# Kernel tuning notes

Measured on AMD Instinct MI355X. Metric: run time of the kernel, lower is better.

The kernel has to match this reference:

```python
import jax, jax.numpy as jnp
import numpy as np

B = 32768
IN = 2
H = 512
OUT = 1
OM = 128   # output_module_size
HG = 128   # halt_gate_size
MAX_ITER = 32
EPS = 1e-3


def _w(k, shape, fan_in):
    bound = 1.0 / np.sqrt(fan_in)
    return jax.random.uniform(k, shape, jnp.float32, -bound, bound)


def setup_inputs() -> dict:
    key = jax.random.key(0)
    ks = jax.random.split(key, 32)
    d = {"x": jax.random.normal(ks[0], (B, IN), jnp.float32)}
    # four LSTM gates: input Linear(IN,H) and hidden Linear(H,H), each with bias
    names = ["i", "f", "c", "o"]
    for j, g in enumerate(names):
        d[f"W{g}_x"] = _w(ks[1 + 4 * j], (IN, H), IN)
        d[f"b{g}_x"] = _w(ks[2 + 4 * j], (H,), IN)
        d[f"W{g}_h"] = _w(ks[3 + 4 * j], (H, H), H)
        d[f"b{g}_h"] = _w(ks[4 + 4 * j], (H,), H)
    # halt gate: Linear(H,HG) -> ReLU -> Linear(HG,1) -> Sigmoid
    d["halt_W1"] = _w(ks[17], (H, HG), H)
    d["halt_b1"] = _w(ks[18], (HG,), H)
    d["halt_W2"] = _w(ks[19], (HG, 1), HG)
    d["halt_b2"] = _w(ks[20], (1,), HG)
    # output module: Linear(H,OM) -> ReLU -> Linear(OM,OM) -> Linear(OM,OUT) -> Sigmoid
    d["out_W1"] = _w(ks[21], (H, OM), H)
    d["out_b1"] = _w(ks[22], (OM,), H)
    d["out_W2"] = _w(ks[23], (OM, OM), OM)
    d["out_b2"] = _w(ks[24], (OM,), OM)
    d["out_W3"] = _w(ks[25], (OM, OUT), OM)
    d["out_b3"] = _w(ks[26], (OUT,), OM)
    return d


def _act_forward(x, Wi_x, bi_x, Wi_h, bi_h, Wf_x, bf_x, Wf_h, bf_h,
                 Wc_x, bc_x, Wc_h, bc_h, Wo_x, bo_x, Wo_h, bo_h,
                 halt_W1, halt_b1, halt_W2, halt_b2,
                 out_W1, out_b1, out_W2, out_b2, out_W3, out_b3):
    b = x.shape[0]
    # input projections are iteration-invariant: precompute once
    xi = x @ Wi_x + bi_x
    xf = x @ Wf_x + bf_x
    xc = x @ Wc_x + bc_x
    xo = x @ Wo_x + bo_x

    def step(carry, t):
        state, cell, p_sum, active, acc = carry
        i_g = jax.nn.sigmoid(xi + state @ Wi_h + bi_h)
        f_g = jax.nn.sigmoid(xf + state @ Wf_h + bf_h)
        c_g = jnp.tanh(xc + state @ Wc_h + bc_h)
        o_g = jax.nn.sigmoid(xo + state @ Wo_h + bo_h)
        am = active[:, None]
        new_cell = jnp.where(am, f_g * cell + i_g * c_g, cell)
        new_state = jnp.where(am, o_g * jnp.tanh(new_cell), state)
        # output head (inactive rows contribute zero weight below)
        h1 = jax.nn.relu(new_state @ out_W1 + out_b1)
        out = jax.nn.sigmoid((h1 @ out_W2 + out_b2) @ out_W3 + out_b3)  # [B,OUT]
        # halt probability
        hh = jax.nn.relu(new_state @ halt_W1 + halt_b1)
        halt = jax.nn.sigmoid(hh @ halt_W2 + halt_b2)[:, 0]  # [B]
        halt = jnp.where(active, halt, 0.0)
        p_new = p_sum + halt
        is_last = t == (MAX_ITER - 1)
        finished = (p_new >= 1.0 - EPS) | is_last
        adj = active & finished
        halt_adj = jnp.where(adj, halt + (1.0 - p_new), halt)
        p_new = jnp.where(adj, 1.0, p_new)
        acc = acc + out * halt_adj[:, None]
        active_new = active & jnp.logical_not(finished)
        return (new_state, new_cell, p_new, active_new, acc), None

    init = (
        jnp.zeros((b, H), jnp.float32),   # state
        jnp.zeros((b, H), jnp.float32),   # cell
        jnp.zeros((b,), jnp.float32),     # p_sum
        jnp.ones((b,), bool),             # active
        jnp.zeros((b, OUT), jnp.float32), # weighted-output accumulator
    )
    (state, cell, p_sum, active, acc), _ = jax.lax.scan(step, init, jnp.arange(MAX_ITER))
    return acc


def reference(x, Wi_x, bi_x, Wi_h, bi_h, Wf_x, bf_x, Wf_h, bf_h,
              Wc_x, bc_x, Wc_h, bc_h, Wo_x, bo_x, Wo_h, bo_h,
              halt_W1, halt_b1, halt_W2, halt_b2,
              out_W1, out_b1, out_W2, out_b2, out_W3, out_b3):
    return _act_forward(x, Wi_x, bi_x, Wi_h, bi_h, Wf_x, bf_x, Wf_h, bf_h,
                        Wc_x, bc_x, Wc_h, bc_h, Wo_x, bo_x, Wo_h, bo_h,
                        halt_W1, halt_b1, halt_W2, halt_b2,
                        out_W1, out_b1, out_W2, out_b2, out_W3, out_b3)
```

## Files before the change

### kernel.cpp

```cpp
#include <hip/hip_runtime.h>
#include <hip/hip_bf16.h>

#define KD   544
#define ASTR 552
#define RPB  64
#define THR  512

typedef __bf16 bf8 __attribute__((ext_vector_type(8)));
typedef float f32x4 __attribute__((ext_vector_type(4)));

__device__ __forceinline__ float sigm(float x)  { return 1.0f / (1.0f + __expf(-x)); }
__device__ __forceinline__ float tanh_(float x) { return 2.0f / (1.0f + __expf(-2.0f * x)) - 1.0f; }

__global__ void pack_whT(const float* __restrict__ Wi_h, const float* __restrict__ Wf_h,
                         const float* __restrict__ Wc_h, const float* __restrict__ Wo_h,
                         const float* __restrict__ Wi_x, const float* __restrict__ Wf_x,
                         const float* __restrict__ Wc_x, const float* __restrict__ Wo_x,
                         const float* __restrict__ bi_x, const float* __restrict__ bf_x,
                         const float* __restrict__ bc_x, const float* __restrict__ bo_x,
                         const float* __restrict__ bi_h, const float* __restrict__ bf_h,
                         const float* __restrict__ bc_h, const float* __restrict__ bo_h,
                         __bf16* __restrict__ whT)
{
  int idx = blockIdx.x * 256 + threadIdx.x;
  if (idx >= 2048 * KD) return;
  int j = idx / KD, k = idx % KD;
  int g = j >> 9, c = j & 511;
  const float* Wh = (g == 0) ? Wi_h : (g == 1) ? Wf_h : (g == 2) ? Wc_h : Wo_h;
  const float* Wx = (g == 0) ? Wi_x : (g == 1) ? Wf_x : (g == 2) ? Wc_x : Wo_x;
  const float* bx = (g == 0) ? bi_x : (g == 1) ? bf_x : (g == 2) ? bc_x : bo_x;
  const float* bh = (g == 0) ? bi_h : (g == 1) ? bf_h : (g == 2) ? bc_h : bo_h;
  float v = 0.0f;
  if (k < 512)       v = Wh[k * 512 + c];
  else if (k == 512) v = Wx[c];
  else if (k == 513) v = Wx[512 + c];
  else if (k == 514) v = bx[c] + bh[c];
  whT[idx] = (__bf16)v;
}

__global__ void pack_w1cat(const float* __restrict__ outW1, const float* __restrict__ outb1,
                           const float* __restrict__ haltW1, const float* __restrict__ haltb1,
                           __bf16* __restrict__ w1cat)
{
  int idx = blockIdx.x * 256 + threadIdx.x;
  if (idx >= 256 * KD) return;
  int j = idx / KD, k = idx % KD;
  float v = 0.0f;
  if (j < 128) {
    if (k < 512)       v = outW1[k * 128 + j];
    else if (k == 514) v = outb1[j];
  } else {
    int jj = j - 128;
    if (k < 512)       v = haltW1[k * 128 + jj];
    else if (k == 514) v = haltb1[jj];
  }
  w1cat[idx] = (__bf16)v;
}

__global__ void pack_w23(const float* __restrict__ outW2, const float* __restrict__ outb2,
                         const float* __restrict__ outW3, const float* __restrict__ outb3,
                         float* __restrict__ w23, float* __restrict__ b23)
{
  int c1 = threadIdx.x;
  float s = 0.0f;
  for (int c2 = 0; c2 < 128; ++c2) s += outW2[c1 * 128 + c2] * outW3[c2];
  w23[c1] = s;
  if (c1 == 0) {
    float b = 0.0f;
    for (int c2 = 0; c2 < 128; ++c2) b += outb2[c2] * outW3[c2];
    b23[0] = b + outb3[0];
  }
}

__global__ __launch_bounds__(THR, 2) void act_main(
    const float* __restrict__ x,
    const __bf16* __restrict__ whT,
    const __bf16* __restrict__ w1cat,
    const float* __restrict__ w23,
    const float* __restrict__ b23p,
    const float* __restrict__ haltW2,
    const float* __restrict__ haltb2,
    float* __restrict__ out)
{
  __shared__ __align__(16) __bf16 Abuf[2][RPB][ASTR];
  __shared__ float wv[256];
  __shared__ float partials[8][RPB];
  __shared__ int anyact_s;

  const int tid  = threadIdx.x;
  const int wave = tid >> 6;
  const int lane = tid & 63;
  const int lg   = lane >> 4;
  const int lc   = lane & 15;
  const int row0 = blockIdx.x * RPB;

  if (tid < 256) wv[tid] = (tid < 128) ? w23[tid] : haltW2[tid - 128];
  for (int idx = tid; idx < 2 * RPB * ASTR; idx += THR) {
    int b = idx / (RPB * ASTR);
    int rem = idx - b * (RPB * ASTR);
    int r = rem / ASTR;
    int k = rem - r * ASTR;
    float v = 0.0f;
    if (k == 512)      v = x[(row0 + r) * 2 + 0];
    else if (k == 513) v = x[(row0 + r) * 2 + 1];
    else if (k == 514) v = 1.0f;
    Abuf[b][r][k] = (__bf16)v;
  }
  if (tid == 0) anyact_s = 1;
  __syncthreads();

  float cell[4][4][4];
#pragma unroll
  for (int n = 0; n < 4; ++n)
#pragma unroll
    for (int m = 0; m < 4; ++m)
#pragma unroll
      for (int q = 0; q < 4; ++q) cell[n][m][q] = 0.0f;

  bool  active = (tid < 64);
  float p_sum = 0.0f, accum = 0.0f;
  const float b23 = b23p[0];
  const float bh2 = haltb2[0];
  const f32x4 zero4 = {0.0f, 0.0f, 0.0f, 0.0f};

  int cur = 0;
  for (int t = 0; t < 32; ++t) {
    const int kstart = (t == 0) ? 16 : 0;
#pragma unroll
    for (int n = 0; n < 4; ++n) {
      const int colb = wave * 64 + n * 16 + lc;
      const __bf16* bp0 = whT + (size_t)(colb)        * KD + lg * 8;
      const __bf16* bp1 = whT + (size_t)(512  + colb) * KD + lg * 8;
      const __bf16* bp2 = whT + (size_t)(1024 + colb) * KD + lg * 8;
      const __bf16* bp3 = whT + (size_t)(1536 + colb) * KD + lg * 8;
      f32x4 acc[4][4];
#pragma unroll
      for (int g = 0; g < 4; ++g)
#pragma unroll
        for (int m = 0; m < 4; ++m) acc[g][m] = zero4;

      bf8 b0 = *(const bf8*)(bp0 + kstart * 32);
      bf8 b1 = *(const bf8*)(bp1 + kstart * 32);
      bf8 b2 = *(const bf8*)(bp2 + kstart * 32);
      bf8 b3 = *(const bf8*)(bp3 + kstart * 32);
#pragma unroll 1
      for (int kk = kstart; kk < 16; ++kk) {
        bf8 av[4];
#pragma unroll
        for (int m = 0; m < 4; ++m)
          av[m] = *(const bf8*)&Abuf[cur][m * 16 + lc][kk * 32 + lg * 8];
        bf8 nb0 = *(const bf8*)(bp0 + (kk + 1) * 32);
        bf8 nb1 = *(const bf8*)(bp1 + (kk + 1) * 32);
        bf8 nb2 = *(const bf8*)(bp2 + (kk + 1) * 32);
        bf8 nb3 = *(const bf8*)(bp3 + (kk + 1) * 32);
#pragma unroll
        for (int m = 0; m < 4; ++m) {
          acc[0][m] = __builtin_amdgcn_mfma_f32_16x16x32_bf16(av[m], b0, acc[0][m], 0, 0, 0);
          acc[1][m] = __builtin_amdgcn_mfma_f32_16x16x32_bf16(av[m], b1, acc[1][m], 0, 0, 0);
          acc[2][m] = __builtin_amdgcn_mfma_f32_16x16x32_bf16(av[m], b2, acc[2][m], 0, 0, 0);
          acc[3][m] = __builtin_amdgcn_mfma_f32_16x16x32_bf16(av[m], b3, acc[3][m], 0, 0, 0);
        }
        b0 = nb0; b1 = nb1; b2 = nb2; b3 = nb3;
      }
      {
        bf8 av[4];
#pragma unroll
        for (int m = 0; m < 4; ++m)
          av[m] = *(const bf8*)&Abuf[cur][m * 16 + lc][16 * 32 + lg * 8];
#pragma unroll
        for (int m = 0; m < 4; ++m) {
          acc[0][m] = __builtin_amdgcn_mfma_f32_16x16x32_bf16(av[m], b0, acc[0][m], 0, 0, 0);
          acc[1][m] = __builtin_amdgcn_mfma_f32_16x16x32_bf16(av[m], b1, acc[1][m], 0, 0, 0);
          acc[2][m] = __builtin_amdgcn_mfma_f32_16x16x32_bf16(av[m], b2, acc[2][m], 0, 0, 0);
          acc[3][m] = __builtin_amdgcn_mfma_f32_16x16x32_bf16(av[m], b3, acc[3][m], 0, 0, 0);
        }
      }
#pragma unroll
      for (int m = 0; m < 4; ++m) {
#pragma unroll
        for (int q = 0; q < 4; ++q) {
          float iv = sigm(acc[0][m][q]);
          float fv = sigm(acc[1][m][q]);
          float cv = tanh_(acc[2][m][q]);
          float ov = sigm(acc[3][m][q]);
          float cn = fv * cell[n][m][q] + iv * cv;
          cell[n][m][q] = cn;
          float h = ov * tanh_(cn);
          Abuf[cur ^ 1][m * 16 + lg * 4 + q][colb] = (__bf16)h;
        }
      }
    }
    __syncthreads();
    {
      const int jb0 = wave * 32 + lc;
      const __bf16* hp0 = w1cat + (size_t)jb0        * KD + lg * 8;
      const __bf16* hp1 = w1cat + (size_t)(jb0 + 16) * KD + lg * 8;
      f32x4 hacc[2][4];
#pragma unroll
      for (int n2 = 0; n2 < 2; ++n2)
#pragma unroll
        for (int m = 0; m < 4; ++m) hacc[n2][m] = zero4;
      bf8 hb0 = *(const bf8*)(hp0);
      bf8 hb1 = *(const bf8*)(hp1);
#pragma unroll 1
      for (int kk = 0; kk < 16; ++kk) {
        bf8 av[4];
#pragma unroll
        for (int m = 0; m < 4; ++m)
          av[m] = *(const bf8*)&Abuf[cur ^ 1][m * 16 + lc][kk * 32 + lg * 8];
        bf8 nb0 = *(const bf8*)(hp0 + (kk + 1) * 32);
        bf8 nb1 = *(const bf8*)(hp1 + (kk + 1) * 32);
#pragma unroll
        for (int m = 0; m < 4; ++m) {
          hacc[0][m] = __builtin_amdgcn_mfma_f32_16x16x32_bf16(av[m], hb0, hacc[0][m], 0, 0, 0);
          hacc[1][m] = __builtin_amdgcn_mfma_f32_16x16x32_bf16(av[m], hb1, hacc[1][m], 0, 0, 0);
        }
        hb0 = nb0; hb1 = nb1;
      }
      {
        bf8 av[4];
#pragma unroll
        for (int m = 0; m < 4; ++m)
          av[m] = *(const bf8*)&Abuf[cur ^ 1][m * 16 + lc][16 * 32 + lg * 8];
#pragma unroll
        for (int m = 0; m < 4; ++m) {
          hacc[0][m] = __builtin_amdgcn_mfma_f32_16x16x32_bf16(av[m], hb0, hacc[0][m], 0, 0, 0);
          hacc[1][m] = __builtin_amdgcn_mfma_f32_16x16x32_bf16(av[m], hb1, hacc[1][m], 0, 0, 0);
        }
      }
      const float wv0 = wv[wave * 32 + lc];
      const float wv1 = wv[wave * 32 + 16 + lc];
#pragma unroll
      for (int m = 0; m < 4; ++m) {
#pragma unroll
        for (int q = 0; q < 4; ++q) {
          float s = fmaxf(hacc[0][m][q], 0.0f) * wv0 + fmaxf(hacc[1][m][q], 0.0f) * wv1;
          s += __shfl_xor(s, 1, 64);
          s += __shfl_xor(s, 2, 64);
          s += __shfl_xor(s, 4, 64);
          s += __shfl_xor(s, 8, 64);
          if (lc == 0) partials[wave][m * 16 + lg * 4 + q] = s;
        }
      }
    }
    __syncthreads();
    if (tid < 64) {
      float od = partials[0][tid] + partials[1][tid] + partials[2][tid] + partials[3][tid] + b23;
      float hd = partials[4][tid] + partials[5][tid] + partials[6][tid] + partials[7][tid] + bh2;
      float outv  = sigm(od);
      float haltv = sigm(hd);
      if (active) {
        float pn  = p_sum + haltv;
        bool  fin = (pn >= 0.999f) || (t == 31);
        accum += outv * (fin ? (haltv + (1.0f - pn)) : haltv);
        p_sum  = fin ? 1.0f : pn;
        active = !fin;
      }
      unsigned long long mk = __ballot(active);
      if (tid == 0) anyact_s = (mk != 0ull) ? 1 : 0;
    }
    __syncthreads();
    if (!anyact_s) break;
    cur ^= 1;
  }
  if (tid < 64) out[row0 + tid] = accum;
}

extern "C" void kernel_launch(void* const* d_in, const int* in_sizes, int n_in,
                              void* d_out, int out_size, void* d_ws, size_t ws_size,
                              hipStream_t stream) {
  const float* x     = (const float*)d_in[0];
  const float* Wi_x  = (const float*)d_in[1];
  const float* bi_x  = (const float*)d_in[2];
  const float* Wi_h  = (const float*)d_in[3];
  const float* bi_h  = (const float*)d_in[4];
  const float* Wf_x  = (const float*)d_in[5];
  const float* bf_x  = (const float*)d_in[6];
  const float* Wf_h  = (const float*)d_in[7];
  const float* bf_h  = (const float*)d_in[8];
  const float* Wc_x  = (const float*)d_in[9];
  const float* bc_x  = (const float*)d_in[10];
  const float* Wc_h  = (const float*)d_in[11];
  const float* bc_h  = (const float*)d_in[12];
  const float* Wo_x  = (const float*)d_in[13];
  const float* bo_x  = (const float*)d_in[14];
  const float* Wo_h  = (const float*)d_in[15];
  const float* bo_h  = (const float*)d_in[16];
  const float* hW1   = (const float*)d_in[17];
  const float* hb1   = (const float*)d_in[18];
  const float* hW2   = (const float*)d_in[19];
  const float* hb2   = (const float*)d_in[20];
  const float* oW1   = (const float*)d_in[21];
  const float* ob1   = (const float*)d_in[22];
  const float* oW2   = (const float*)d_in[23];
  const float* ob2   = (const float*)d_in[24];
  const float* oW3   = (const float*)d_in[25];
  const float* ob3   = (const float*)d_in[26];

  __bf16* whT   = (__bf16*)d_ws;
  __bf16* w1cat = whT + (size_t)2048 * KD;
  float*  w23   = (float*)(w1cat + (size_t)256 * KD);
  float*  b23   = w23 + 128;

  pack_whT<<<dim3((2048 * KD + 255) / 256), dim3(256), 0, stream>>>(
      Wi_h, Wf_h, Wc_h, Wo_h, Wi_x, Wf_x, Wc_x, Wo_x,
      bi_x, bf_x, bc_x, bo_x, bi_h, bf_h, bc_h, bo_h, whT);
  pack_w1cat<<<dim3((256 * KD + 255) / 256), dim3(256), 0, stream>>>(oW1, ob1, hW1, hb1, w1cat);
  pack_w23<<<dim3(1), dim3(128), 0, stream>>>(oW2, ob2, oW3, ob3, w23, b23);
  act_main<<<dim3(32768 / RPB), dim3(THR), 0, stream>>>(
      x, whT, w1cat, w23, b23, hW2, hb2, (float*)d_out);
}
```

Before: 424.8 us.

## Split ACT loop into two passes, compacting still-active rows after early steps

The recurrent loop is split into two kernels. The first runs the first few steps for all rows, then uses an atomic counter to compact rows that are still active and spills their state and cell (bf16), p_sum, accumulator and original index to workspace. The second pass runs the remaining steps only on the compacted rows, so blocks whose rows have mostly halted no longer waste matrix work, and blocks past the active count exit immediately. The three pack kernels are also merged into one launch. The cost is extra global traffic for the spill and reload, bf16 rounding of the cell state, and an extra launch.

```diff
diff --git a/kernel.cpp b/kernel.cpp
--- a/kernel.cpp
+++ b/kernel.cpp
@@ -5,6 +5,8 @@
 #define ASTR 552
 #define RPB  64
 #define THR  512
+#define T1   3
+#define NROW 32768
 
 typedef __bf16 bf8 __attribute__((ext_vector_type(8)));
 typedef float f32x4 __attribute__((ext_vector_type(4)));
@@ -12,7 +14,7 @@
 __device__ __forceinline__ float sigm(float x)  { return 1.0f / (1.0f + __expf(-x)); }
 __device__ __forceinline__ float tanh_(float x) { return 2.0f / (1.0f + __expf(-2.0f * x)) - 1.0f; }
 
-__global__ void pack_whT(const float* __restrict__ Wi_h, const float* __restrict__ Wf_h,
+__global__ void pack_all(const float* __restrict__ Wi_h, const float* __restrict__ Wf_h,
                          const float* __restrict__ Wc_h, const float* __restrict__ Wo_h,
                          const float* __restrict__ Wi_x, const float* __restrict__ Wf_x,
                          const float* __restrict__ Wc_x, const float* __restrict__ Wo_x,
@@ -20,59 +22,60 @@
                          const float* __restrict__ bc_x, const float* __restrict__ bo_x,
                          const float* __restrict__ bi_h, const float* __restrict__ bf_h,
                          const float* __restrict__ bc_h, const float* __restrict__ bo_h,
-                         __bf16* __restrict__ whT)
+                         const float* __restrict__ outW1, const float* __restrict__ outb1,
+                         const float* __restrict__ haltW1, const float* __restrict__ haltb1,
+                         const float* __restrict__ outW2, const float* __restrict__ outb2,
+                         const float* __restrict__ outW3, const float* __restrict__ outb3,
+                         __bf16* __restrict__ whT, __bf16* __restrict__ w1cat,
+                         float* __restrict__ w23, float* __restrict__ b23,
+                         int* __restrict__ cntp)
 {
-  int idx = blockIdx.x * 256 + threadIdx.x;
-  if (idx >= 2048 * KD) return;
-  int j = idx / KD, k = idx % KD;
-  int g = j >> 9, c = j & 511;
-  const float* Wh = (g == 0) ? Wi_h : (g == 1) ? Wf_h : (g == 2) ? Wc_h : Wo_h;
-  const float* Wx = (g == 0) ? Wi_x : (g == 1) ? Wf_x : (g == 2) ? Wc_x : Wo_x;
-  const float* bx = (g == 0) ? bi_x : (g == 1) ? bf_x : (g == 2) ? bc_x : bo_x;
-  const float* bh = (g == 0) ? bi_h : (g == 1) ? bf_h : (g == 2) ? bc_h : bo_h;
-  float v = 0.0f;
-  if (k < 512)       v = Wh[k * 512 + c];
-  else if (k == 512) v = Wx[c];
-  else if (k == 513) v = Wx[512 + c];
-  else if (k == 514) v = bx[c] + bh[c];
-  whT[idx] = (__bf16)v;
+  int b = blockIdx.x;
+  if (b < 4352) {
+    int idx = b * 256 + threadIdx.x;
+    int j = idx / KD, k = idx % KD;
+    int g = j >> 9, c = j & 511;
+    const float* Wh = (g == 0) ? Wi_h : (g == 1) ? Wf_h : (g == 2) ? Wc_h : Wo_h;
+    const float* Wx = (g == 0) ? Wi_x : (g == 1) ? Wf_x : (g == 2) ? Wc_x : Wo_x;
+    const float* bx = (g == 0) ? bi_x : (g == 1) ? bf_x : (g == 2) ? bc_x : bo_x;
+    const float* bh = (g == 0) ? bi_h : (g == 1) ? bf_h : (g == 2) ? bc_h : bo_h;
+    float v = 0.0f;
+    if (k < 512)       v = Wh[k * 512 + c];
+    else if (k == 512) v = Wx[c];
+    else if (k == 513) v = Wx[512 + c];
+    else if (k == 514) v = bx[c] + bh[c];
+    whT[idx] = (__bf16)v;
+  } else if (b < 4896) {
+    int idx = (b - 4352) * 256 + threadIdx.x;
+    int j = idx / KD, k = idx % KD;
+    float v = 0.0f;
+    if (j < 128) {
+      if (k < 512)       v = outW1[k * 128 + j];
+      else if (k == 514) v = outb1[j];
+    } else {
+      int jj = j - 128;
+      if (k < 512)       v = haltW1[k * 128 + jj];
+      else if (k == 514) v = haltb1[jj];
+    }
+    w1cat[idx] = (__bf16)v;
+  } else {
+    int c1 = threadIdx.x;
+    if (c1 < 128) {
+      float s = 0.0f;
+      for (int c2 = 0; c2 < 128; ++c2) s += outW2[c1 * 128 + c2] * outW3[c2];
+      w23[c1] = s;
+    }
+    if (c1 == 0) {
+      float bb = 0.0f;
+      for (int c2 = 0; c2 < 128; ++c2) bb += outb2[c2] * outW3[c2];
+      b23[0] = bb + outb3[0];
+      cntp[0] = 0;
+    }
+  }
 }
 
-__global__ void pack_w1cat(const float* __restrict__ outW1, const float* __restrict__ outb1,
-                           const float* __restrict__ haltW1, const float* __restrict__ haltb1,
-                           __bf16* __restrict__ w1cat)
-{
-  int idx = blockIdx.x * 256 + threadIdx.x;
-  if (idx >= 256 * KD) return;
-  int j = idx / KD, k = idx % KD;
-  float v = 0.0f;
-  if (j < 128) {
-    if (k < 512)       v = outW1[k * 128 + j];
-    else if (k == 514) v = outb1[j];
-  } else {
-    int jj = j - 128;
-    if (k < 512)       v = haltW1[k * 128 + jj];
-    else if (k == 514) v = haltb1[jj];
-  }
-  w1cat[idx] = (__bf16)v;
-}
-
-__global__ void pack_w23(const float* __restrict__ outW2, const float* __restrict__ outb2,
-                         const float* __restrict__ outW3, const float* __restrict__ outb3,
-                         float* __restrict__ w23, float* __restrict__ b23)
-{
-  int c1 = threadIdx.x;
-  float s = 0.0f;
-  for (int c2 = 0; c2 < 128; ++c2) s += outW2[c1 * 128 + c2] * outW3[c2];
-  w23[c1] = s;
-  if (c1 == 0) {
-    float b = 0.0f;
-    for (int c2 = 0; c2 < 128; ++c2) b += outb2[c2] * outW3[c2];
-    b23[0] = b + outb3[0];
-  }
-}
-
-__global__ __launch_bounds__(THR, 2) void act_main(
+template<bool P1>
+__global__ __launch_bounds__(THR, 2) void act_pass(
     const float* __restrict__ x,
     const __bf16* __restrict__ whT,
     const __bf16* __restrict__ w1cat,
@@ -80,12 +83,26 @@
     const float* __restrict__ b23p,
     const float* __restrict__ haltW2,
     const float* __restrict__ haltb2,
+    __bf16* __restrict__ sstate,
+    __bf16* __restrict__ scell,
+    float* __restrict__ spsum,
+    float* __restrict__ saccum,
+    int* __restrict__ sidx,
+    int* __restrict__ cntp,
     float* __restrict__ out)
 {
+  int cnt_v = 0, sbase = 0;
+  if constexpr (!P1) {
+    cnt_v = cntp[0];
+    sbase = blockIdx.x * RPB;
+    if (sbase >= cnt_v) return;
+  }
+
   __shared__ __align__(16) __bf16 Abuf[2][RPB][ASTR];
   __shared__ float wv[256];
   __shared__ float partials[8][RPB];
   __shared__ int anyact_s;
+  __shared__ int rowslot[RPB];
 
   const int tid  = threadIdx.x;
   const int wave = tid >> 6;
@@ -95,37 +112,90 @@
   const int row0 = blockIdx.x * RPB;
 
   if (tid < 256) wv[tid] = (tid < 128) ? w23[tid] : haltW2[tid - 128];
-  for (int idx = tid; idx < 2 * RPB * ASTR; idx += THR) {
-    int b = idx / (RPB * ASTR);
-    int rem = idx - b * (RPB * ASTR);
-    int r = rem / ASTR;
-    int k = rem - r * ASTR;
-    float v = 0.0f;
-    if (k == 512)      v = x[(row0 + r) * 2 + 0];
-    else if (k == 513) v = x[(row0 + r) * 2 + 1];
-    else if (k == 514) v = 1.0f;
-    Abuf[b][r][k] = (__bf16)v;
+
+  if constexpr (P1) {
+    for (int w = tid; w < 2 * RPB * 69; w += THR) {
+      int bb  = w / (RPB * 69);
+      int rem = w - bb * (RPB * 69);
+      int r   = rem / 69;
+      int j   = rem - r * 69;
+      bf8 v;
+#pragma unroll
+      for (int e = 0; e < 8; ++e) v[e] = (__bf16)0.0f;
+      if (j == 64) {
+        v[0] = (__bf16)x[(row0 + r) * 2 + 0];
+        v[1] = (__bf16)x[(row0 + r) * 2 + 1];
+        v[2] = (__bf16)1.0f;
+      }
+      *(bf8*)&Abuf[bb][r][j * 8] = v;
+    }
+  } else {
+    for (int w = tid; w < RPB * 68; w += THR) {
+      int r = w / 68, j = w - r * 68;
+      int slot = sbase + r;
+      bf8 v;
+#pragma unroll
+      for (int e = 0; e < 8; ++e) v[e] = (__bf16)0.0f;
+      if (slot < cnt_v) v = *(const bf8*)(sstate + (size_t)slot * KD + j * 8);
+      *(bf8*)&Abuf[0][r][j * 8] = v;
+      if (j >= 64) *(bf8*)&Abuf[1][r][j * 8] = v;
+    }
+    for (int w = tid; w < RPB * 64; w += THR) {
+      int r = w / 64, j = w - r * 64;
+      int slot = sbase + r;
+      bf8 v;
+#pragma unroll
+      for (int e = 0; e < 8; ++e) v[e] = (__bf16)0.0f;
+      if (slot < cnt_v) v = *(const bf8*)(scell + (size_t)slot * 512 + j * 8);
+      *(bf8*)&Abuf[1][r][j * 8] = v;
+    }
   }
   if (tid == 0) anyact_s = 1;
   __syncthreads();
 
   float cell[4][4][4];
-#pragma unroll
-  for (int n = 0; n < 4; ++n)
-#pragma unroll
-    for (int m = 0; m < 4; ++m)
-#pragma unroll
-      for (int q = 0; q < 4; ++q) cell[n][m][q] = 0.0f;
-
-  bool  active = (tid < 64);
-  float p_sum = 0.0f, accum = 0.0f;
+  if constexpr (P1) {
+#pragma unroll
+    for (int n = 0; n < 4; ++n)
+#pragma unroll
+      for (int m = 0; m < 4; ++m)
+#pragma unroll
+        for (int q = 0; q < 4; ++q) cell[n][m][q] = 0.0f;
+  } else {
+#pragma unroll
+    for (int n = 0; n < 4; ++n)
+#pragma unroll
+      for (int m = 0; m < 4; ++m)
+#pragma unroll
+        for (int q = 0; q < 4; ++q)
+          cell[n][m][q] = (float)Abuf[1][m * 16 + lg * 4 + q][wave * 64 + n * 16 + lc];
+  }
+
+  bool  valid, active;
+  float p_sum, accum;
+  int   oidx;
+  if constexpr (P1) {
+    valid = (tid < 64); active = valid;
+    p_sum = 0.0f; accum = 0.0f; oidx = row0 + tid;
+  } else {
+    int slot = sbase + tid;
+    valid = (tid < 64) && (slot < cnt_v);
+    active = valid;
+    p_sum = valid ? spsum[slot]  : 1.0f;
+    accum = valid ? saccum[slot] : 0.0f;
+    oidx  = valid ? sidx[slot]   : 0;
+    __syncthreads();
+  }
+
   const float b23 = b23p[0];
   const float bh2 = haltb2[0];
   const f32x4 zero4 = {0.0f, 0.0f, 0.0f, 0.0f};
 
   int cur = 0;
-  for (int t = 0; t < 32; ++t) {
-    const int kstart = (t == 0) ? 16 : 0;
+  const int T0 = P1 ? 0 : T1;
+  const int TE = P1 ? T1 : 32;
+  for (int t = T0; t < TE; ++t) {
+    const int kstart = (P1 && t == 0) ? 16 : 0;
 #pragma unroll
     for (int n = 0; n < 4; ++n) {
       const int colb = wave * 64 + n * 16 + lc;
@@ -263,7 +333,50 @@
     if (!anyact_s) break;
     cur ^= 1;
   }
-  if (tid < 64) out[row0 + tid] = accum;
+
+  if constexpr (P1) {
+    if (tid < 64) {
+      unsigned long long mk = __ballot(active);
+      int base = 0;
+      if (lane == 0 && mk) base = atomicAdd(cntp, __popcll(mk));
+      base = __shfl(base, 0, 64);
+      int rank = __popcll(mk & ((1ull << lane) - 1ull));
+      int slot = active ? (base + rank) : -1;
+      rowslot[tid] = slot;
+      if (active) {
+        spsum[slot]  = p_sum;
+        saccum[slot] = accum;
+        sidx[slot]   = oidx;
+      } else {
+        out[oidx] = accum;
+      }
+      if (tid == 0) anyact_s = (mk != 0ull) ? 1 : 0;
+    }
+    __syncthreads();
+    if (anyact_s) {
+#pragma unroll
+      for (int n = 0; n < 4; ++n)
+#pragma unroll
+        for (int m = 0; m < 4; ++m)
+#pragma unroll
+          for (int q = 0; q < 4; ++q)
+            Abuf[cur ^ 1][m * 16 + lg * 4 + q][wave * 64 + n * 16 + lc] = (__bf16)cell[n][m][q];
+      __syncthreads();
+      for (int w = tid; w < RPB * 132; w += THR) {
+        int r = w / 132, j = w - r * 132;
+        int slot = rowslot[r];
+        if (slot < 0) continue;
+        if (j < 68)
+          *(bf8*)(sstate + (size_t)slot * KD + j * 8) = *(const bf8*)&Abuf[cur][r][j * 8];
+        else {
+          int jj = j - 68;
+          *(bf8*)(scell + (size_t)slot * 512 + jj * 8) = *(const bf8*)&Abuf[cur ^ 1][r][jj * 8];
+        }
+      }
+    }
+  } else {
+    if (valid) out[oidx] = accum;
+  }
 }
 
 extern "C" void kernel_launch(void* const* d_in, const int* in_sizes, int n_in,
@@ -297,16 +410,27 @@
   const float* oW3   = (const float*)d_in[25];
   const float* ob3   = (const float*)d_in[26];
 
-  __bf16* whT   = (__bf16*)d_ws;
-  __bf16* w1cat = whT + (size_t)2048 * KD;
-  float*  w23   = (float*)(w1cat + (size_t)256 * KD);
-  float*  b23   = w23 + 128;
-
-  pack_whT<<<dim3((2048 * KD + 255) / 256), dim3(256), 0, stream>>>(
+  char* p = (char*)d_ws;
+  __bf16* whT   = (__bf16*)p;                       p += (size_t)2048 * KD * 2;
+  __bf16* w1cat = (__bf16*)p;                       p += (size_t)256 * KD * 2;
+  float*  w23   = (float*)p;                        p += 512;
+  float*  b23   = (float*)p;                        p += 16;
+  int*    cnt   = (int*)p;                          p += 240;
+  __bf16* sstate= (__bf16*)p;                       p += (size_t)NROW * KD * 2;
+  __bf16* scell = (__bf16*)p;                       p += (size_t)NROW * 512 * 2;
+  float*  spsum = (float*)p;                        p += (size_t)NROW * 4;
+  float*  saccum= (float*)p;                        p += (size_t)NROW * 4;
+  int*    sidx  = (int*)p;                          p += (size_t)NROW * 4;
+
+  pack_all<<<dim3(4897), dim3(256), 0, stream>>>(
       Wi_h, Wf_h, Wc_h, Wo_h, Wi_x, Wf_x, Wc_x, Wo_x,
-      bi_x, bf_x, bc_x, bo_x, bi_h, bf_h, bc_h, bo_h, whT);
-  pack_w1cat<<<dim3((256 * KD + 255) / 256), dim3(256), 0, stream>>>(oW1, ob1, hW1, hb1, w1cat);
-  pack_w23<<<dim3(1), dim3(128), 0, stream>>>(oW2, ob2, oW3, ob3, w23, b23);
-  act_main<<<dim3(32768 / RPB), dim3(THR), 0, stream>>>(
-      x, whT, w1cat, w23, b23, hW2, hb2, (float*)d_out);
+      bi_x, bf_x, bc_x, bo_x, bi_h, bf_h, bc_h, bo_h,
+      oW1, ob1, hW1, hb1, oW2, ob2, oW3, ob3,
+      whT, w1cat, w23, b23, cnt);
+  act_pass<true><<<dim3(NROW / RPB), dim3(THR), 0, stream>>>(
+      x, whT, w1cat, w23, b23, hW2, hb2,
+      sstate, scell, spsum, saccum, sidx, cnt, (float*)d_out);
+  act_pass<false><<<dim3(NROW / RPB), dim3(THR), 0, stream>>>(
+      x, whT, w1cat, w23, b23, hW2, hb2,
+      sstate, scell, spsum, saccum, sidx, cnt, (float*)d_out);
 }
```

Result: faster. 407.3 us (-4.1%).
